# Kernel tuning notes

Hardware: AMD Instinct MI355X
Metric: run time of the kernel (lower is better)

## Reference

```python
import jax, jax.numpy as jnp
import numpy as np

TEMPERATURE = 0.1  # from __init__ temperature
NEG_INF = -1e30


def setup_inputs() -> dict:
    key = jax.random.key(0)
    k1, k2, k3, k4, k5 = jax.random.split(key, 5)
    B, D = 8192, 128
    return {
        "zis": jax.random.normal(k1, (B, D), dtype=jnp.float32),
        "zjs": jax.random.normal(k2, (B, D), dtype=jnp.float32),
        "ilabels": jax.random.randint(k3, (B,), 0, 100, dtype=jnp.int64),
        "jlabels": jax.random.randint(k4, (B,), 0, 100, dtype=jnp.int64),
        "weights": jax.random.uniform(k5, (B,), dtype=jnp.float32),
        "idx": 0,
    }


def reference(zis, zjs, ilabels, jlabels, weights, idx):
    B = zjs.shape[0]
    # forward F.normalize + cosine_matrix's normalize is idempotent -> single L2 normalize
    zi = zis / jnp.linalg.norm(zis, axis=1, keepdims=True)
    zj = zjs / jnp.linalg.norm(zjs, axis=1, keepdims=True)
    # similarity_matrix = 1 - (1 - zj @ zi^T); rows indexed by zjs
    logits = (zj @ zi.T) / TEMPERATURE  # [B, B]
    # labels[i, j] = (ilabels[j] == jlabels[i])
    labels = ilabels[None, :] == jlabels[:, None]  # [B, B] bool
    neg_mask = ~labels  # 'zeros' columns per row
    rows = jnp.arange(B)
    pos_idx = idx + rows  # class_level=False: ones = idx + i, size = 1
    pos = logits[rows, pos_idx]  # [B]
    # CrossEntropy over cat([pos, logits[i, zeros]]) at label 0:
    # loss_i = logsumexp([pos_i, neg_row_i]) - pos_i (numerically stable)
    neg_max = jnp.max(jnp.where(neg_mask, logits, NEG_INF), axis=1)
    m = jnp.maximum(pos, neg_max)  # [B]
    denom = jnp.exp(pos - m) + jnp.sum(
        jnp.where(neg_mask, jnp.exp(logits - m[:, None]), 0.0), axis=1
    )
    loss = m + jnp.log(denom) - pos  # [B]
    # size==1 path: loss*w / w (faithful to torch weighted sum / weight.sum())
    w = weights[pos_idx]
    loss = (loss * w) / w
    return jnp.sum(loss) / B
```

## Files before the change

### kernel.cpp

```cpp
#include <hip/hip_runtime.h>


#define BB 8192
#define DD 128
#define CP 256
#define RSL 512
#define NGR 16

typedef __attribute__((ext_vector_type(8))) short short8;
typedef __attribute__((ext_vector_type(4))) float floatx4;

#define GLOBAL_AS __attribute__((address_space(1)))
#define LDS_AS    __attribute__((address_space(3)))

static __device__ __forceinline__ float wave_sum(float v) {
#pragma unroll
    for (int off = 32; off > 0; off >>= 1) v += __shfl_xor(v, off, 64);
    return v;
}

static __device__ __forceinline__ unsigned short f2bf(float f) {
    unsigned int u = __float_as_uint(f);
    return (unsigned short)((u + 0x7FFFu + ((u >> 16) & 1u)) >> 16);
}

__global__ __launch_bounds__(256) void prep_kernel(
    const float* __restrict__ zis, const float* __restrict__ zjs,
    unsigned short* __restrict__ Zib, unsigned short* __restrict__ Zjb,
    float* __restrict__ rni, float* __restrict__ rnj,
    float* __restrict__ denom, float* __restrict__ out, int nout)
{
    if (threadIdx.x < 2) denom[blockIdx.x * 2 + threadIdx.x] = 0.0f;
    if (blockIdx.x == 0 && (int)threadIdx.x < nout) out[threadIdx.x] = 0.0f;

    int wave = threadIdx.x >> 6, lane = threadIdx.x & 63;
    int row = blockIdx.x * 4 + wave;
    const float* src; unsigned short* dst; float* rn; int r;
    if (row < BB) { src = zis; dst = Zib; rn = rni; r = row; }
    else          { src = zjs; dst = Zjb; rn = rnj; r = row - BB; }
    float2 u = *(const float2*)(src + (size_t)r * DD + lane * 2);
    float s = wave_sum(u.x * u.x + u.y * u.y);
    float sc = 1.0f / sqrtf(s);
    if (lane == 0) rn[r] = sc;
    ushort2 o; o.x = f2bf(u.x * sc); o.y = f2bf(u.y * sc);
    *(ushort2*)(dst + (size_t)r * DD + lane * 2) = o;
}

__global__ __launch_bounds__(512, 2) void panel_kernel(
    const unsigned short* __restrict__ Zjb,
    const unsigned short* __restrict__ Zib,
    const int* __restrict__ ilab, const int* __restrict__ jlab,
    float* __restrict__ denom)
{
    __shared__ __align__(16) unsigned short Bp[CP * DD];

    int tid  = threadIdx.x;
    int lane = tid & 63, wave = tid >> 6;
    int quad = lane >> 4, l15 = lane & 15;
    int c0    = blockIdx.y * CP;
    int rbase = blockIdx.x * RSL;

    {
        int nl = wave * 4 + quad;
        int s  = l15 ^ (nl & 15);
        const unsigned short* gp0 = Zib + (size_t)(c0 + nl) * DD + s * 8;
#pragma unroll
        for (int u = 0; u < 8; ++u) {
            const unsigned short* gp = gp0 + (size_t)u * 32 * DD;
            unsigned short* lp = &Bp[(u * 8 + wave) * 512];
            __builtin_amdgcn_global_load_lds((const GLOBAL_AS void*)gp,
                                             (LDS_AS void*)lp, 16, 0, 0);
        }
    }
    asm volatile("s_waitcnt vmcnt(0)" ::: "memory");
    __builtin_amdgcn_s_barrier();

    int ilv[NGR];
#pragma unroll
    for (int g = 0; g < NGR; ++g) ilv[g] = ilab[c0 + g * 16 + l15];

#pragma unroll
    for (int c = 0; c < 2; ++c) {
        int r0 = rbase + wave * 64 + c * 32;

        short8 af[2][4];
#pragma unroll
        for (int mt = 0; mt < 2; ++mt)
#pragma unroll
            for (int ks = 0; ks < 4; ++ks)
                af[mt][ks] = *(const short8*)(Zjb
                    + (size_t)(r0 + mt * 16 + l15) * DD + ks * 32 + quad * 8);

        int jrv[8];
#pragma unroll
        for (int mt = 0; mt < 2; ++mt)
#pragma unroll
            for (int r = 0; r < 4; ++r)
                jrv[mt * 4 + r] = jlab[r0 + mt * 16 + quad * 4 + r];

        float rs[2][4];
#pragma unroll
        for (int mt = 0; mt < 2; ++mt)
#pragma unroll
            for (int r = 0; r < 4; ++r) rs[mt][r] = 0.0f;

        auto GRAN = [&](int g, floatx4 (&a)[2]) {
            const unsigned short* rb = &Bp[(g * 16 + l15) * DD];
            short8 b[4];
#pragma unroll
            for (int ks = 0; ks < 4; ++ks)
                b[ks] = *(const short8*)(rb + (((ks * 4 + quad) ^ l15) * 8));
            floatx4 zz = (floatx4){0.f, 0.f, 0.f, 0.f};
            a[0] = __builtin_amdgcn_mfma_f32_16x16x32_bf16(af[0][0], b[0], zz, 0, 0, 0);
            a[1] = __builtin_amdgcn_mfma_f32_16x16x32_bf16(af[1][0], b[0], zz, 0, 0, 0);
#pragma unroll
            for (int ks = 1; ks < 4; ++ks) {
                a[0] = __builtin_amdgcn_mfma_f32_16x16x32_bf16(af[0][ks], b[ks], a[0], 0, 0, 0);
                a[1] = __builtin_amdgcn_mfma_f32_16x16x32_bf16(af[1][ks], b[ks], a[1], 0, 0, 0);
            }
        };
        auto EPI = [&](floatx4 (&a)[2], int il) {
#pragma unroll
            for (int mt = 0; mt < 2; ++mt)
#pragma unroll
                for (int r = 0; r < 4; ++r) {
                    float e = __expf(fmaf(a[mt][r], 10.0f, -10.0f));
                    rs[mt][r] += (il != jrv[mt * 4 + r]) ? e : 0.0f;
                }
        };

        floatx4 accA[2], accB[2];
        accB[0] = (floatx4){-1e30f, -1e30f, -1e30f, -1e30f};
        accB[1] = accB[0];
        int ilB = 0;

        __builtin_amdgcn_s_setprio(1);
#pragma unroll
        for (int g = 0; g < NGR; g += 2) {
            GRAN(g,     accA); EPI(accB, ilB);
            GRAN(g + 1, accB); EPI(accA, ilv[g]);
            ilB = ilv[g + 1];
        }
        __builtin_amdgcn_s_setprio(0);
        EPI(accB, ilB);

#pragma unroll
        for (int mt = 0; mt < 2; ++mt)
#pragma unroll
            for (int r = 0; r < 4; ++r) {
                float v = rs[mt][r];
                v += __shfl_xor(v, 1, 64);
                v += __shfl_xor(v, 2, 64);
                v += __shfl_xor(v, 4, 64);
                v += __shfl_xor(v, 8, 64);
                if (l15 == 0)
                    atomicAdd(&denom[r0 + mt * 16 + quad * 4 + r], v);
            }
    }
}

__global__ __launch_bounds__(256) void posfinal_kernel(
    const float* __restrict__ zis, const float* __restrict__ zjs,
    const float* __restrict__ rni, const float* __restrict__ rnj,
    const float* __restrict__ denom, const float* __restrict__ wts,
    const int* __restrict__ idxp, float* __restrict__ out)
{
    int wave = threadIdx.x >> 6, lane = threadIdx.x & 63;
    int idx = idxp[0];
    float ll = 0.0f;
#pragma unroll
    for (int t = 0; t < 4; ++t) {
        int i = blockIdx.x * 16 + wave * 4 + t;
        int j = idx + i;
        float2 a  = *(const float2*)(zjs + (size_t)i * DD + lane * 2);
        float2 b2 = *(const float2*)(zis + (size_t)j * DD + lane * 2);
        float s = wave_sum(a.x * b2.x + a.y * b2.y);
        if (lane == 0) {
            float p = s * rni[j] * rnj[i] * 10.0f;
            float l = 10.0f + logf(__expf(p - 10.0f) + denom[i]) - p;
            float w = wts[j];
            ll += (l * w) / w;
        }
    }
    __shared__ float part[4];
    if (lane == 0) part[wave] = ll;
    __syncthreads();
    if (threadIdx.x == 0)
        atomicAdd(out, (part[0] + part[1] + part[2] + part[3]) * (1.0f / BB));
}

extern "C" void kernel_launch(void* const* d_in, const int* in_sizes, int n_in,
                              void* d_out, int out_size, void* d_ws, size_t ws_size,
                              hipStream_t stream) {
    const float* zis = (const float*)d_in[0];
    const float* zjs = (const float*)d_in[1];
    const int* ilab = (const int*)d_in[2];
    const int* jlab = (const int*)d_in[3];
    const float* wts = (const float*)d_in[4];
    const int* idxp = (const int*)d_in[5];
    float* out = (float*)d_out;

    float* rni   = (float*)d_ws;
    float* rnj   = rni + BB;
    float* denom = rnj + BB;
    unsigned short* Zib = (unsigned short*)(denom + BB);
    unsigned short* Zjb = Zib + (size_t)BB * DD;

    prep_kernel<<<2 * BB / 4, 256, 0, stream>>>(
        zis, zjs, Zib, Zjb, rni, rnj, denom, out, out_size);
    panel_kernel<<<dim3(BB / RSL, BB / CP), 512, 0, stream>>>(
        Zjb, Zib, ilab, jlab, denom);
    posfinal_kernel<<<BB / 16, 256, 0, stream>>>(
        zis, zjs, rni, rnj, denom, wts, idxp, out);
}
```

Before: 116.8 us.

## Drop manual MFMA/epilogue ping-pong, stage labels in LDS, use native exp2

Replaces the two-accumulator software pipeline, which overlapped one granule's MFMAs with the previous granule's exp epilogue, with a single accumulator and a straight loop, leaving interleaving to the compiler. Column labels are staged once per block into LDS and read per granule instead of being held in 16 registers per thread. The exponential becomes a direct exp2 with the log2(e) factor folded into the FMA. The aim is lower register pressure and fewer instructions, at the cost of losing explicit MFMA/VALU overlap.

```diff
diff --git a/kernel.cpp b/kernel.cpp
--- a/kernel.cpp
+++ b/kernel.cpp
@@ -12,6 +12,8 @@
 
 #define GLOBAL_AS __attribute__((address_space(1)))
 #define LDS_AS    __attribute__((address_space(3)))
+
+#define L2E10 14.4269504088896340f
 
 static __device__ __forceinline__ float wave_sum(float v) {
 #pragma unroll
@@ -53,6 +55,7 @@
     float* __restrict__ denom)
 {
     __shared__ __align__(16) unsigned short Bp[CP * DD];
+    __shared__ int Il[CP];
 
     int tid  = threadIdx.x;
     int lane = tid & 63, wave = tid >> 6;
@@ -72,12 +75,9 @@
                                              (LDS_AS void*)lp, 16, 0, 0);
         }
     }
-    asm volatile("s_waitcnt vmcnt(0)" ::: "memory");
+    if (tid < CP) Il[tid] = ilab[c0 + tid];
+    asm volatile("s_waitcnt vmcnt(0) lgkmcnt(0)" ::: "memory");
     __builtin_amdgcn_s_barrier();
-
-    int ilv[NGR];
-#pragma unroll
-    for (int g = 0; g < NGR; ++g) ilv[g] = ilab[c0 + g * 16 + l15];
 
 #pragma unroll
     for (int c = 0; c < 2; ++c) {
@@ -104,45 +104,37 @@
 #pragma unroll
             for (int r = 0; r < 4; ++r) rs[mt][r] = 0.0f;
 
-        auto GRAN = [&](int g, floatx4 (&a)[2]) {
+        floatx4 acc[2];
+        int iln = Il[l15];
+
+        __builtin_amdgcn_s_setprio(1);
+#pragma unroll
+        for (int g = 0; g < NGR; ++g) {
             const unsigned short* rb = &Bp[(g * 16 + l15) * DD];
             short8 b[4];
 #pragma unroll
             for (int ks = 0; ks < 4; ++ks)
                 b[ks] = *(const short8*)(rb + (((ks * 4 + quad) ^ l15) * 8));
             floatx4 zz = (floatx4){0.f, 0.f, 0.f, 0.f};
-            a[0] = __builtin_amdgcn_mfma_f32_16x16x32_bf16(af[0][0], b[0], zz, 0, 0, 0);
-            a[1] = __builtin_amdgcn_mfma_f32_16x16x32_bf16(af[1][0], b[0], zz, 0, 0, 0);
+            acc[0] = __builtin_amdgcn_mfma_f32_16x16x32_bf16(af[0][0], b[0], zz, 0, 0, 0);
+            acc[1] = __builtin_amdgcn_mfma_f32_16x16x32_bf16(af[1][0], b[0], zz, 0, 0, 0);
 #pragma unroll
             for (int ks = 1; ks < 4; ++ks) {
-                a[0] = __builtin_amdgcn_mfma_f32_16x16x32_bf16(af[0][ks], b[ks], a[0], 0, 0, 0);
-                a[1] = __builtin_amdgcn_mfma_f32_16x16x32_bf16(af[1][ks], b[ks], a[1], 0, 0, 0);
+                acc[0] = __builtin_amdgcn_mfma_f32_16x16x32_bf16(af[0][ks], b[ks], acc[0], 0, 0, 0);
+                acc[1] = __builtin_amdgcn_mfma_f32_16x16x32_bf16(af[1][ks], b[ks], acc[1], 0, 0, 0);
             }
-        };
-        auto EPI = [&](floatx4 (&a)[2], int il) {
+            int ilc = iln;
+            if (g + 1 < NGR) iln = Il[(g + 1) * 16 + l15];
 #pragma unroll
             for (int mt = 0; mt < 2; ++mt)
 #pragma unroll
                 for (int r = 0; r < 4; ++r) {
-                    float e = __expf(fmaf(a[mt][r], 10.0f, -10.0f));
-                    rs[mt][r] += (il != jrv[mt * 4 + r]) ? e : 0.0f;
+                    float e = __builtin_amdgcn_exp2f(
+                        fmaf(acc[mt][r], L2E10, -L2E10));
+                    rs[mt][r] += (ilc != jrv[mt * 4 + r]) ? e : 0.0f;
                 }
-        };
-
-        floatx4 accA[2], accB[2];
-        accB[0] = (floatx4){-1e30f, -1e30f, -1e30f, -1e30f};
-        accB[1] = accB[0];
-        int ilB = 0;
-
-        __builtin_amdgcn_s_setprio(1);
-#pragma unroll
-        for (int g = 0; g < NGR; g += 2) {
-            GRAN(g,     accA); EPI(accB, ilB);
-            GRAN(g + 1, accB); EPI(accA, ilv[g]);
-            ilB = ilv[g + 1];
         }
         __builtin_amdgcn_s_setprio(0);
-        EPI(accB, ilB);
 
 #pragma unroll
         for (int mt = 0; mt < 2; ++mt)
```

Result: faster. 110.7 us (-5.2%).
